# Optimization experiments

Hardware: AMD Instinct MI355X
Metric: run time of the kernel (lower is better)

Reference implementation:

```python
import jax, jax.numpy as jnp
import numpy as np

B = 64       # graphs per batch
NPG = 1000   # nodes per graph
EPG = 8000   # edges per graph
F = 128      # num_node_features


def _lin_w(k, fi, fo):
    s = 1.0 / np.sqrt(fi)
    return jax.random.uniform(k, (fi, fo), jnp.float32, -s, s)


def setup_inputs() -> dict:
    key = jax.random.key(0)
    ks = jax.random.split(key, 40)
    N, E = B * NPG, B * EPG

    def edges(k1, k2):
        src = jax.random.randint(k1, (E,), 0, NPG)
        dst = jax.random.randint(k2, (E,), 0, NPG)
        off = (jnp.arange(E) // EPG) * NPG  # keep edges within each graph
        return jnp.stack([src + off, dst + off]).astype(jnp.int32)

    inp = {
        'x0': jax.random.normal(ks[0], (N, F), jnp.float32),
        'edge_attr0': jax.random.uniform(ks[1], (E, 4), jnp.float32),
        'edge_index0': edges(ks[2], ks[3]),
        'x1': jax.random.normal(ks[4], (N, F), jnp.float32),
        'edge_attr1': jax.random.uniform(ks[5], (E, 4), jnp.float32),
        'edge_index1': edges(ks[6], ks[7]),
        'batch0': (jnp.arange(N) // NPG).astype(jnp.int32),
        'batch1': (jnp.arange(N) // NPG).astype(jnp.int32),
        'num_graphs': B,
    }
    # GCNConv weights/biases (6 convs, all F->F)
    names = ['1A', '1B', '1C', '1D', '2', '3']
    for i, nm in enumerate(names):
        inp['W' + nm] = _lin_w(ks[8 + i], F, F)
        inp['b' + nm] = jnp.zeros((F,), jnp.float32)
    # SAGPooling score GNN (GraphConv: lin_rel with bias, lin_root no bias), 3F -> 1
    inp['Ws_rel'] = _lin_w(ks[20], 3 * F, 1)
    inp['bs_rel'] = jnp.zeros((1,), jnp.float32)
    inp['Ws_root'] = _lin_w(ks[21], 3 * F, 1)
    # MLP: 6F -> 32 -> 8 -> 2
    inp['Wm1'] = _lin_w(ks[22], 6 * F, 32)
    inp['bm1'] = jnp.zeros((32,), jnp.float32)
    inp['Wm2'] = _lin_w(ks[23], 32, 8)
    inp['bm2'] = jnp.zeros((8,), jnp.float32)
    inp['Wm3'] = _lin_w(ks[24], 8, 2)
    inp['bm3'] = jnp.zeros((2,), jnp.float32)
    return inp


def gcn_conv(x, W, b, row, col, ew):
    # PyG GCNConv: add self-loops (w=1), symmetric norm, gather->scatter-add
    N = x.shape[0]
    h = x @ W  # [N, F]
    sl = jnp.arange(N)
    row_f = jnp.concatenate([row, sl])
    col_f = jnp.concatenate([col, sl])
    w_f = jnp.concatenate([ew, jnp.ones((N,), x.dtype)])
    deg = jax.ops.segment_sum(w_f, col_f, num_segments=N)
    dinv = jnp.where(deg > 0, jax.lax.rsqrt(jnp.maximum(deg, 1e-12)), 0.0)
    norm = (dinv[row_f] * w_f * dinv[col_f])[:, None]
    return jax.ops.segment_sum(h[row_f] * norm, col_f, num_segments=N) + b


def reference(x0, edge_attr0, edge_index0, x1, edge_attr1, edge_index1,
              batch0, batch1, num_graphs,
              W1A, b1A, W1B, b1B, W1C, b1C, W1D, b1D, W2, b2, W3, b3,
              Ws_rel, bs_rel, Ws_root, Wm1, bm1, Wm2, bm2, Wm3, bm3):
    Bn = int(num_graphs)

    def branch(x, ea, ei):
        row, col = ei[0], ei[1]
        N = x.shape[0]
        ones_e = jnp.ones((ei.shape[1],), x.dtype)
        xa = jax.nn.relu(gcn_conv(x, W1A, b1A, row, col, ea[:, 0]))
        xb = jax.nn.relu(gcn_conv(x, W1B, b1B, row, col, ea[:, 1]))
        xc = jax.nn.relu(gcn_conv(x, W1C, b1C, row, col, ea[:, 2]))
        xd = jax.nn.relu(gcn_conv(x, W1D, b1D, row, col, ea[:, 3]))
        g1 = (xa + xb + xc + xd) * 0.25
        g2 = jax.nn.relu(gcn_conv(g1, W2, b2, row, col, ones_e))
        g3 = gcn_conv(g2, W3, b3, row, col, ones_e)
        g = jnp.concatenate([g1, g2, g3], axis=1)  # [N, 3F]
        # SAGPooling score via GraphConv (sum aggr, no norm/self-loops)
        agg = jax.ops.segment_sum(g[row], col, num_segments=N)
        score = (agg @ Ws_rel + bs_rel + g @ Ws_root)[:, 0]  # [N]
        npg = N // Bn
        k = npg // 2  # ratio=0.5, even graph size
        sv, si = jax.lax.top_k(score.reshape(Bn, npg), k)
        gg = g.reshape(Bn, npg, g.shape[1])
        sel = jnp.take_along_axis(gg, si[..., None], axis=1)  # [B, k, 3F]
        pooled = sel * jnp.tanh(sv)[..., None]
        return pooled.mean(axis=1)  # global_mean_pool -> [B, 3F]

    r0 = branch(x0, edge_attr0, edge_index0)
    r1 = branch(x1, edge_attr1, edge_index1)
    r = jnp.concatenate([r0, r1], axis=1)  # [B, 6F]
    h = jax.nn.relu(r @ Wm1 + bm1)
    h = jax.nn.relu(h @ Wm2 + bm2)
    return h @ Wm3 + bm3  # [B, 2]
```

## Files before the change

kernel.cpp:

```cpp
#include <hip/hip_runtime.h>
#include <math.h>


#define TPB 256

__device__ __forceinline__ int swz_block(int bid, int nb) {
  int per = bid & 7;
  return per * (nb >> 3) + (bid >> 3);
}

__device__ __forceinline__ void f4fma(float4& a, const float4 b, float s) {
  a.x += b.x * s; a.y += b.y * s; a.z += b.z * s; a.w += b.w * s;
}
__device__ __forceinline__ float4 f4s(const float4 a, float s) {
  return make_float4(a.x * s, a.y * s, a.z * s, a.w * s);
}


__global__ __launch_bounds__(TPB) void count2_k(const int* __restrict__ ec0,
                                                const int* __restrict__ ec1,
                                                int* __restrict__ cnt, int E) {
  int e = blockIdx.x * TPB + threadIdx.x;
  if (e < 2 * E) {
    int br = e >= E;
    int el = e - br * E;
    int c = br ? ec1[el] : ec0[el];
    atomicAdd(&cnt[br * (gridDim.x * 0 + 0) + 0 + c + br * 64000], 1);
  }
}

__global__ __launch_bounds__(512) void scan1_k(const int* __restrict__ cnt,
                                               int* __restrict__ rowptr,
                                               int* __restrict__ bsum, int tn) {
  __shared__ int s[512];
  int tid = threadIdx.x;
  int gid = blockIdx.x * 512 + tid;
  int v = (gid < tn) ? cnt[gid] : 0;
  s[tid] = v;
  __syncthreads();
  for (int o = 1; o < 512; o <<= 1) {
    int t = (tid >= o) ? s[tid - o] : 0;
    __syncthreads();
    s[tid] += t;
    __syncthreads();
  }
  if (gid < tn) rowptr[gid] = s[tid] - v;
  if (tid == 511) bsum[blockIdx.x] = s[511];
}

__global__ __launch_bounds__(TPB) void scan2_k(int* __restrict__ bsum, int nb) {
  __shared__ int s[TPB];
  int tid = threadIdx.x;
  int v = (tid < nb) ? bsum[tid] : 0;
  s[tid] = v;
  __syncthreads();
  for (int o = 1; o < TPB; o <<= 1) {
    int t = (tid >= o) ? s[tid - o] : 0;
    __syncthreads();
    s[tid] += t;
    __syncthreads();
  }
  if (tid < nb) bsum[tid] = s[tid] - v;
}

__global__ __launch_bounds__(512) void scan3_k(int* __restrict__ rowptr,
                                               const int* __restrict__ bsum,
                                               int tn, int tE) {
  int gid = blockIdx.x * 512 + threadIdx.x;
  if (gid < tn) rowptr[gid] += bsum[blockIdx.x];
  if (gid == 0) rowptr[tn] = tE;
}

__global__ __launch_bounds__(TPB) void fill2_k(const int* __restrict__ ec0,
                                               const int* __restrict__ ec1,
                                               const int* __restrict__ rowptr,
                                               int* __restrict__ fil,
                                               int* __restrict__ csr, int N,
                                               int E) {
  int e = blockIdx.x * TPB + threadIdx.x;
  if (e < 2 * E) {
    int br = e >= E;
    int el = e - br * E;
    int c = (br ? ec1[el] : ec0[el]) + br * N;
    int p = rowptr[c] + atomicAdd(&fil[c], 1);
    csr[p] = e;
  }
}

__global__ __launch_bounds__(TPB) void sortadj_k(const int* __restrict__ rowptr,
                                                 int* __restrict__ csr, int tn) {
  int i = blockIdx.x * TPB + threadIdx.x;
  if (i >= tn) return;
  int s = rowptr[i], e = rowptr[i + 1];
  for (int a = s + 1; a < e; ++a) {
    int v = csr[a];
    int b = a - 1;
    while (b >= s && csr[b] > v) { csr[b + 1] = csr[b]; --b; }
    csr[b + 1] = v;
  }
}

__global__ __launch_bounds__(TPB) void deg2_k(const int* __restrict__ rowptr,
                                              const int* __restrict__ csr,
                                              const float* __restrict__ ea0,
                                              const float* __restrict__ ea1,
                                              float* __restrict__ dinv, int N,
                                              int E) {
  int i = blockIdx.x * TPB + threadIdx.x;
  int tn = 2 * N;
  if (i >= tn) return;
  int br = i >= N;
  const float* ea = br ? ea1 : ea0;
  int ebase = br * E;
  int s = rowptr[i], e = rowptr[i + 1];
  float d0 = 1.f, d1 = 1.f, d2 = 1.f, d3 = 1.f;
  for (int j = s; j < e; ++j) {
    int el = csr[j] - ebase;
    float4 w = *reinterpret_cast<const float4*>(&ea[(size_t)el * 4]);
    d0 += w.x; d1 += w.y; d2 += w.z; d3 += w.w;
  }
  float dO = (float)(e - s) + 1.f;
  dinv[0 * tn + i] = 1.f / sqrtf(d0);
  dinv[1 * tn + i] = 1.f / sqrtf(d1);
  dinv[2 * tn + i] = 1.f / sqrtf(d2);
  dinv[3 * tn + i] = 1.f / sqrtf(d3);
  dinv[4 * tn + i] = 1.f / sqrtf(dO);
}

__global__ __launch_bounds__(TPB) void eresolve2_k(
    const int* __restrict__ csr, const int* __restrict__ er0,
    const int* __restrict__ er1, const float* __restrict__ ea0,
    const float* __restrict__ ea1, const float* __restrict__ dinv, int N,
    int E, int* __restrict__ csrSrc, float4* __restrict__ csrW,
    float* __restrict__ csrWO) {
  int j = blockIdx.x * TPB + threadIdx.x;
  if (j >= 2 * E) return;
  int br = j >= E;
  int tn = 2 * N;
  int el = csr[j] - br * E;
  int rl = br ? er1[el] : er0[el];
  int gi = br * N + rl;
  const float* ea = br ? ea1 : ea0;
  float4 a = *reinterpret_cast<const float4*>(&ea[(size_t)el * 4]);
  csrSrc[j] = rl;
  csrW[j] = make_float4(a.x * dinv[gi], a.y * dinv[tn + gi],
                        a.z * dinv[2 * tn + gi], a.w * dinv[3 * tn + gi]);
  csrWO[j] = dinv[4 * tn + gi];
}

__global__ __launch_bounds__(256) void gather4_k(
    const float4* __restrict__ X, const int* __restrict__ rowptr_b,
    const int* __restrict__ csrSrc, const float4* __restrict__ csrW,
    const float* __restrict__ dinvp, int tn, float4* __restrict__ S0,
    float4* __restrict__ S1, float4* __restrict__ S2, float4* __restrict__ S3) {
  int sb = swz_block(blockIdx.x, gridDim.x);
  int node = sb * 8 + (threadIdx.x >> 5);
  int l = threadIdx.x & 31;
  int s = rowptr_b[node], e = rowptr_b[node + 1];
  float d0 = dinvp[node], d1 = dinvp[tn + node], d2 = dinvp[2 * tn + node],
        d3 = dinvp[3 * tn + node];
  float4 xs = X[(size_t)node * 32 + l];
  float4 a0 = f4s(xs, d0), a1 = f4s(xs, d1), a2 = f4s(xs, d2), a3 = f4s(xs, d3);
  int j = s;
  for (; j + 3 < e; j += 4) {
    int r0 = csrSrc[j], r1 = csrSrc[j + 1], r2 = csrSrc[j + 2], r3 = csrSrc[j + 3];
    float4 w0 = csrW[j], w1 = csrW[j + 1], w2 = csrW[j + 2], w3 = csrW[j + 3];
    float4 x0 = X[(size_t)r0 * 32 + l];
    float4 x1 = X[(size_t)r1 * 32 + l];
    float4 x2 = X[(size_t)r2 * 32 + l];
    float4 x3 = X[(size_t)r3 * 32 + l];
    f4fma(a0, x0, w0.x); f4fma(a1, x0, w0.y); f4fma(a2, x0, w0.z); f4fma(a3, x0, w0.w);
    f4fma(a0, x1, w1.x); f4fma(a1, x1, w1.y); f4fma(a2, x1, w1.z); f4fma(a3, x1, w1.w);
    f4fma(a0, x2, w2.x); f4fma(a1, x2, w2.y); f4fma(a2, x2, w2.z); f4fma(a3, x2, w2.w);
    f4fma(a0, x3, w3.x); f4fma(a1, x3, w3.y); f4fma(a2, x3, w3.z); f4fma(a3, x3, w3.w);
  }
  for (; j < e; ++j) {
    int r = csrSrc[j];
    float4 w = csrW[j];
    float4 xr = X[(size_t)r * 32 + l];
    f4fma(a0, xr, w.x); f4fma(a1, xr, w.y); f4fma(a2, xr, w.z); f4fma(a3, xr, w.w);
  }
  size_t o = (size_t)node * 32 + l;
  S0[o] = f4s(a0, d0);
  S1[o] = f4s(a1, d1);
  S2[o] = f4s(a2, d2);
  S3[o] = f4s(a3, d3);
}

__global__ __launch_bounds__(256) void gather1_k(
    const float4* __restrict__ X, const int* __restrict__ rowptr_b,
    const int* __restrict__ csrSrc, const float* __restrict__ csrWO,
    const float* __restrict__ dinvO, int N, float4* __restrict__ Out) {
  int sb = swz_block(blockIdx.x, gridDim.x);
  int node = sb * 8 + (threadIdx.x >> 5);
  int l = threadIdx.x & 31;
  int s = rowptr_b[node], e = rowptr_b[node + 1];
  float di = dinvO[node];
  float4 acc = f4s(X[(size_t)node * 32 + l], di);
  int j = s;
  for (; j + 3 < e; j += 4) {
    int r0 = csrSrc[j], r1 = csrSrc[j + 1], r2 = csrSrc[j + 2], r3 = csrSrc[j + 3];
    float w0 = csrWO[j], w1 = csrWO[j + 1], w2 = csrWO[j + 2], w3 = csrWO[j + 3];
    float4 x0 = X[(size_t)r0 * 32 + l];
    float4 x1 = X[(size_t)r1 * 32 + l];
    float4 x2 = X[(size_t)r2 * 32 + l];
    float4 x3 = X[(size_t)r3 * 32 + l];
    f4fma(acc, x0, w0); f4fma(acc, x1, w1); f4fma(acc, x2, w2); f4fma(acc, x3, w3);
  }
  for (; j < e; ++j) {
    f4fma(acc, X[(size_t)csrSrc[j] * 32 + l], csrWO[j]);
  }
  Out[(size_t)node * 32 + l] = f4s(acc, di);
}

template <bool RELU>
__global__ __launch_bounds__(256) void gemm_epi(const float* __restrict__ A,
                                                const float* __restrict__ W,
                                                const float* __restrict__ bias,
                                                float* __restrict__ C, int M) {
  __shared__ float As[64][64];
  __shared__ float Ws[64][128];
  int tid = threadIdx.x;
  int tx = tid & 31;
  int ty = tid >> 5;
  int rowBase = blockIdx.x * 64;
  float acc[8][4] = {};
  for (int kc = 0; kc < 128; kc += 64) {
#pragma unroll
    for (int i = 0; i < 4; ++i) {
      int idx = tid + i * 256;
      int r = idx >> 4;
      int c4 = idx & 15;
      *reinterpret_cast<float4*>(&As[r][c4 * 4]) =
          *reinterpret_cast<const float4*>(&A[(size_t)(rowBase + r) * 128 + kc + c4 * 4]);
    }
#pragma unroll
    for (int i = 0; i < 8; ++i) {
      int idx = tid + i * 256;
      int r = idx >> 5;
      int c4 = idx & 31;
      *reinterpret_cast<float4*>(&Ws[r][c4 * 4]) =
          *reinterpret_cast<const float4*>(&W[(size_t)(kc + r) * 128 + c4 * 4]);
    }
    __syncthreads();
#pragma unroll 4
    for (int k = 0; k < 64; ++k) {
      float b0[4];
      *reinterpret_cast<float4*>(b0) = *reinterpret_cast<const float4*>(&Ws[k][tx * 4]);
#pragma unroll
      for (int j = 0; j < 8; ++j) {
        float a = As[ty * 8 + j][k];
        acc[j][0] += a * b0[0];
        acc[j][1] += a * b0[1];
        acc[j][2] += a * b0[2];
        acc[j][3] += a * b0[3];
      }
    }
    __syncthreads();
  }
  float4 bq = *reinterpret_cast<const float4*>(&bias[tx * 4]);
#pragma unroll
  for (int j = 0; j < 8; ++j) {
    float v0 = acc[j][0] + bq.x, v1 = acc[j][1] + bq.y, v2 = acc[j][2] + bq.z,
          v3 = acc[j][3] + bq.w;
    if (RELU) {
      v0 = fmaxf(v0, 0.f); v1 = fmaxf(v1, 0.f); v2 = fmaxf(v2, 0.f); v3 = fmaxf(v3, 0.f);
    }
    size_t r = (size_t)(rowBase + ty * 8 + j) * 128 + tx * 4;
    *reinterpret_cast<float4*>(&C[r]) = make_float4(v0, v1, v2, v3);
  }
}

__global__ __launch_bounds__(256) void gemm4_k(
    const float* __restrict__ S0, const float* __restrict__ S1,
    const float* __restrict__ S2, const float* __restrict__ S3,
    const float* __restrict__ W0, const float* __restrict__ W1,
    const float* __restrict__ W2, const float* __restrict__ W3,
    const float* __restrict__ B0, const float* __restrict__ B1,
    const float* __restrict__ B2, const float* __restrict__ B3,
    float* __restrict__ g1, int tileBase) {
  __shared__ float As[64][64];
  __shared__ float Ws[64][128];
  const float* Sarr[4] = {S0, S1, S2, S3};
  const float* Warr[4] = {W0, W1, W2, W3};
  const float* Barr[4] = {B0, B1, B2, B3};
  int tid = threadIdx.x;
  int tx = tid & 31;
  int ty = tid >> 5;
  int rowBase = (tileBase + blockIdx.x) * 64;
  float facc[8][4] = {};
#pragma unroll
  for (int q = 0; q < 4; ++q) {
    const float* A = Sarr[q];
    const float* W = Warr[q];
    float acc[8][4] = {};
    for (int kc = 0; kc < 128; kc += 64) {
#pragma unroll
      for (int i = 0; i < 4; ++i) {
        int idx = tid + i * 256;
        int r = idx >> 4;
        int c4 = idx & 15;
        *reinterpret_cast<float4*>(&As[r][c4 * 4]) =
            *reinterpret_cast<const float4*>(&A[(size_t)(rowBase + r) * 128 + kc + c4 * 4]);
      }
#pragma unroll
      for (int i = 0; i < 8; ++i) {
        int idx = tid + i * 256;
        int r = idx >> 5;
        int c4 = idx & 31;
        *reinterpret_cast<float4*>(&Ws[r][c4 * 4]) =
            *reinterpret_cast<const float4*>(&W[(size_t)(kc + r) * 128 + c4 * 4]);
      }
      __syncthreads();
#pragma unroll 4
      for (int k = 0; k < 64; ++k) {
        float b0[4];
        *reinterpret_cast<float4*>(b0) = *reinterpret_cast<const float4*>(&Ws[k][tx * 4]);
#pragma unroll
        for (int j = 0; j < 8; ++j) {
          float a = As[ty * 8 + j][k];
          acc[j][0] += a * b0[0];
          acc[j][1] += a * b0[1];
          acc[j][2] += a * b0[2];
          acc[j][3] += a * b0[3];
        }
      }
      __syncthreads();
    }
    float4 bq = *reinterpret_cast<const float4*>(&Barr[q][tx * 4]);
#pragma unroll
    for (int j = 0; j < 8; ++j) {
      facc[j][0] += fmaxf(acc[j][0] + bq.x, 0.f) * 0.25f;
      facc[j][1] += fmaxf(acc[j][1] + bq.y, 0.f) * 0.25f;
      facc[j][2] += fmaxf(acc[j][2] + bq.z, 0.f) * 0.25f;
      facc[j][3] += fmaxf(acc[j][3] + bq.w, 0.f) * 0.25f;
    }
  }
#pragma unroll
  for (int j = 0; j < 8; ++j) {
    size_t r = (size_t)(rowBase + ty * 8 + j) * 128 + tx * 4;
    *reinterpret_cast<float4*>(&g1[r]) =
        make_float4(facc[j][0], facc[j][1], facc[j][2], facc[j][3]);
  }
}

__global__ __launch_bounds__(256) void score_a(
    const float* __restrict__ g1, const float* __restrict__ g2,
    const float* __restrict__ g3, const float* __restrict__ Wrel,
    const float* __restrict__ Wroot, float* __restrict__ trel,
    float* __restrict__ troot, int N) {
  int wave = threadIdx.x >> 6;
  int lane = threadIdx.x & 63;
  int node = blockIdx.x * 4 + wave;
  if (node >= N) return;
  float sr = 0.f, so = 0.f;
#pragma unroll
  for (int t = 0; t < 2; ++t) {
    int f = lane + t * 64;
    float v1 = g1[(size_t)node * 128 + f];
    float v2 = g2[(size_t)node * 128 + f];
    float v3 = g3[(size_t)node * 128 + f];
    sr += v1 * Wrel[f] + v2 * Wrel[128 + f] + v3 * Wrel[256 + f];
    so += v1 * Wroot[f] + v2 * Wroot[128 + f] + v3 * Wroot[256 + f];
  }
  for (int off = 32; off; off >>= 1) {
    sr += __shfl_down(sr, off);
    so += __shfl_down(so, off);
  }
  if (lane == 0) { trel[node] = sr; troot[node] = so; }
}

__global__ __launch_bounds__(TPB) void score_b(
    const int* __restrict__ rowptr_b, const int* __restrict__ csrSrc,
    const float* __restrict__ trel, const float* __restrict__ troot,
    const float* __restrict__ bs, float* __restrict__ score, int N) {
  int i = blockIdx.x * TPB + threadIdx.x;
  if (i >= N) return;
  float sc = bs[0] + troot[i];
  int s = rowptr_b[i], e = rowptr_b[i + 1];
  for (int j = s; j < e; ++j) sc += trel[csrSrc[j]];
  score[i] = sc;
}

__global__ __launch_bounds__(512) void topk_pool(
    const float* __restrict__ score, const float* __restrict__ g1,
    const float* __restrict__ g2, const float* __restrict__ g3,
    float* __restrict__ r, int half, int npg, int k) {
  __shared__ float key[1024];
  __shared__ int idx[1024];
  __shared__ float wts[512];
  int b = blockIdx.x;
  int tid = threadIdx.x;
  int base = b * npg;
  for (int i = tid; i < 1024; i += 512) {
    key[i] = (i < npg) ? score[base + i] : -3.0e38f;
    idx[i] = i;
  }
  __syncthreads();
  for (int kk = 2; kk <= 1024; kk <<= 1) {
    for (int j = kk >> 1; j > 0; j >>= 1) {
      for (int i = tid; i < 1024; i += 512) {
        int ixj = i ^ j;
        if (ixj > i) {
          bool desc = ((i & kk) == 0);
          float ki = key[i], kj = key[ixj];
          bool sw = desc ? (ki < kj) : (ki > kj);
          if (sw) {
            key[i] = kj; key[ixj] = ki;
            int t = idx[i]; idx[i] = idx[ixj]; idx[ixj] = t;
          }
        }
      }
      __syncthreads();
    }
  }
  if (tid < k) wts[tid] = tanhf(key[tid]);
  __syncthreads();
  if (tid < 384) {
    const float* gp = (tid < 128) ? g1 : ((tid < 256) ? g2 : g3);
    int fo = tid & 127;
    float acc = 0.f;
    for (int j = 0; j < k; ++j) {
      int n = base + idx[j];
      acc += wts[j] * gp[(size_t)n * 128 + fo];
    }
    r[(size_t)b * 768 + half * 384 + tid] = acc / (float)k;
  }
}

__global__ __launch_bounds__(64) void mlp_k(
    const float* __restrict__ r, const float* __restrict__ Wm1,
    const float* __restrict__ bm1, const float* __restrict__ Wm2,
    const float* __restrict__ bm2, const float* __restrict__ Wm3,
    const float* __restrict__ bm3, float* __restrict__ out) {
  __shared__ float rr[768];
  __shared__ float h1[32];
  __shared__ float h2[8];
  int b = blockIdx.x;
  int tid = threadIdx.x;
  for (int i = tid; i < 768; i += 64) rr[i] = r[(size_t)b * 768 + i];
  __syncthreads();
  if (tid < 32) {
    float s = bm1[tid];
    for (int i = 0; i < 768; ++i) s += rr[i] * Wm1[i * 32 + tid];
    h1[tid] = fmaxf(s, 0.f);
  }
  __syncthreads();
  if (tid < 8) {
    float s = bm2[tid];
    for (int i = 0; i < 32; ++i) s += h1[i] * Wm2[i * 8 + tid];
    h2[tid] = fmaxf(s, 0.f);
  }
  __syncthreads();
  if (tid < 2) {
    float s = bm3[tid];
    for (int i = 0; i < 8; ++i) s += h2[i] * Wm3[i * 2 + tid];
    out[b * 2 + tid] = s;
  }
}

extern "C" void kernel_launch(void* const* d_in, const int* in_sizes, int n_in,
                              void* d_out, int out_size, void* d_ws, size_t ws_size,
                              hipStream_t stream) {
  const float* x[2]  = {(const float*)d_in[0], (const float*)d_in[3]};
  const float* eat[2] = {(const float*)d_in[1], (const float*)d_in[4]};
  const int*   ei[2] = {(const int*)d_in[2], (const int*)d_in[5]};
  const int N = in_sizes[0] / 128;
  const int E = in_sizes[2] / 2;
  const int tn = 2 * N;
  const int tE = 2 * E;
  const int Bg = 64;
  const int npg = N / Bg;
  const int kq = npg / 2;

  const float* W1[4] = {(const float*)d_in[9], (const float*)d_in[11],
                        (const float*)d_in[13], (const float*)d_in[15]};
  const float* b1[4] = {(const float*)d_in[10], (const float*)d_in[12],
                        (const float*)d_in[14], (const float*)d_in[16]};
  const float* W2 = (const float*)d_in[17];
  const float* b2 = (const float*)d_in[18];
  const float* W3 = (const float*)d_in[19];
  const float* b3 = (const float*)d_in[20];
  const float* Wsrel  = (const float*)d_in[21];
  const float* bsrel  = (const float*)d_in[22];
  const float* Wsroot = (const float*)d_in[23];
  const float* Wm1 = (const float*)d_in[24];
  const float* bm1 = (const float*)d_in[25];
  const float* Wm2 = (const float*)d_in[26];
  const float* bm2 = (const float*)d_in[27];
  const float* Wm3 = (const float*)d_in[28];
  const float* bm3 = (const float*)d_in[29];
  float* out = (float*)d_out;

  char* ws = (char*)d_ws;
  size_t off = 0;
  auto alloc = [&](size_t bytes) -> void* {
    void* p = ws + off;
    off = (off + bytes + 511) & ~(size_t)511;
    return p;
  };
  const size_t nf = (size_t)N * 128 * sizeof(float);
  float* P0 = (float*)alloc(nf);
  float* P1 = (float*)alloc(nf);
  float* P2 = (float*)alloc(nf);
  float* P3 = (float*)alloc(nf);
  float* P4 = (float*)alloc(nf);
  float* dinv = (float*)alloc((size_t)5 * tn * sizeof(float));
  float* trel = (float*)alloc((size_t)N * sizeof(float));
  float* trot = (float*)alloc((size_t)N * sizeof(float));
  float* sco  = (float*)alloc((size_t)N * sizeof(float));
  int* rowptr = (int*)alloc((size_t)(tn + 1) * sizeof(int));
  int* cnt    = (int*)alloc((size_t)tn * sizeof(int));
  int* csr    = (int*)alloc((size_t)tE * sizeof(int));
  int* csrSrc = (int*)alloc((size_t)tE * sizeof(int));
  float4* csrW = (float4*)alloc((size_t)tE * sizeof(float4));
  float* csrWO = (float*)alloc((size_t)tE * sizeof(float));
  int* bsum   = (int*)alloc(1024);
  float* rbuf = (float*)alloc((size_t)Bg * 768 * sizeof(float));
  if (off > ws_size) return;

  const int nbN2 = (tn + TPB - 1) / TPB;
  const int nbE2 = (tE + TPB - 1) / TPB;
  const int nbS  = (tn + 511) / 512;
  const int nbN  = (N + TPB - 1) / TPB;
  const int nbGather = N / 8;
  const int nbGemm = N / 64;
  const int nbGemmHalf = nbGemm / 2;

  hipMemsetAsync(cnt, 0, (size_t)tn * sizeof(int), stream);
  count2_k<<<nbE2, TPB, 0, stream>>>(ei[0] + E, ei[1] + E, cnt, E);
  scan1_k<<<nbS, 512, 0, stream>>>(cnt, rowptr, bsum, tn);
  scan2_k<<<1, TPB, 0, stream>>>(bsum, nbS);
  scan3_k<<<nbS, 512, 0, stream>>>(rowptr, bsum, tn, tE);
  hipMemsetAsync(cnt, 0, (size_t)tn * sizeof(int), stream);
  fill2_k<<<nbE2, TPB, 0, stream>>>(ei[0] + E, ei[1] + E, rowptr, cnt, csr, N, E);
  sortadj_k<<<nbN2, TPB, 0, stream>>>(rowptr, csr, tn);
  deg2_k<<<nbN2, TPB, 0, stream>>>(rowptr, csr, eat[0], eat[1], dinv, N, E);
  eresolve2_k<<<nbE2, TPB, 0, stream>>>(csr, ei[0], ei[1], eat[0], eat[1],
                                        dinv, N, E, csrSrc, csrW, csrWO);

  for (int br = 0; br < 2; ++br) {
    const int* rowptr_b = rowptr + (size_t)br * N;
    const float* dinvp = dinv + (size_t)br * N;
    const float* dinvO = dinv + (size_t)4 * tn + (size_t)br * N;

    gather4_k<<<nbGather, 256, 0, stream>>>(
        (const float4*)x[br], rowptr_b, csrSrc, csrW, dinvp, tn,
        (float4*)P0, (float4*)P1, (float4*)P2, (float4*)P3);
    gemm4_k<<<nbGemmHalf, 256, 0, stream>>>(P0, P1, P2, P3,
                                            W1[0], W1[1], W1[2], W1[3],
                                            b1[0], b1[1], b1[2], b1[3], P4, 0);
    gemm4_k<<<nbGemmHalf, 256, 0, stream>>>(P0, P1, P2, P3,
                                            W1[0], W1[1], W1[2], W1[3],
                                            b1[0], b1[1], b1[2], b1[3], P4,
                                            nbGemmHalf);

    gather1_k<<<nbGather, 256, 0, stream>>>(
        (const float4*)P4, rowptr_b, csrSrc, csrWO, dinvO, N, (float4*)P0);
    gemm_epi<true><<<nbGemm, 256, 0, stream>>>(P0, W2, b2, P1, N);

    gather1_k<<<nbGather, 256, 0, stream>>>(
        (const float4*)P1, rowptr_b, csrSrc, csrWO, dinvO, N, (float4*)P0);
    gemm_epi<false><<<nbGemm, 256, 0, stream>>>(P0, W3, b3, P2, N);

    score_a<<<(N + 3) / 4, 256, 0, stream>>>(P4, P1, P2, Wsrel, Wsroot, trel, trot, N);
    score_b<<<nbN, TPB, 0, stream>>>(rowptr_b, csrSrc, trel, trot, bsrel, sco, N);
    topk_pool<<<Bg, 512, 0, stream>>>(sco, P4, P1, P2, rbuf, br, npg, kq);
  }

  mlp_k<<<Bg, 64, 0, stream>>>(rbuf, Wm1, bm1, Wm2, bm2, Wm3, bm3, out);
}
```

Before: 903.3 us.

## Deepen gather unrolling, split top-k pooling, merge gemm4 launches

Adds an 8-way unrolled edge loop to both gather kernels so more independent row loads are in flight per lane. Splits the top-k pooling kernel into a sort kernel that writes selected indices and tanh weights, and a separate pool kernel launched over graphs by three feature slices with 4-way unrolled gathers, to expose more parallelism than the single 512-thread block per graph. Also merges the two half-grid gemm4 launches into one and cleans up the count kernel's hardcoded offset. Costs extra registers in the gathers plus an additional launch and a small index/weight buffer round trip.

New measurement: 951.4 us. 5.3% more time.

```diff
diff --git a/kernel.cpp b/kernel.cpp
--- a/kernel.cpp
+++ b/kernel.cpp
@@ -5,8 +5,7 @@
 #define TPB 256
 
 __device__ __forceinline__ int swz_block(int bid, int nb) {
-  int per = bid & 7;
-  return per * (nb >> 3) + (bid >> 3);
+  return (bid & 7) * (nb >> 3) + (bid >> 3);
 }
 
 __device__ __forceinline__ void f4fma(float4& a, const float4 b, float s) {
@@ -16,16 +15,16 @@
   return make_float4(a.x * s, a.y * s, a.z * s, a.w * s);
 }
 
-
 __global__ __launch_bounds__(TPB) void count2_k(const int* __restrict__ ec0,
                                                 const int* __restrict__ ec1,
-                                                int* __restrict__ cnt, int E) {
+                                                int* __restrict__ cnt, int N,
+                                                int E) {
   int e = blockIdx.x * TPB + threadIdx.x;
   if (e < 2 * E) {
     int br = e >= E;
     int el = e - br * E;
-    int c = br ? ec1[el] : ec0[el];
-    atomicAdd(&cnt[br * (gridDim.x * 0 + 0) + 0 + c + br * 64000], 1);
+    int c = (br ? ec1[el] : ec0[el]) + br * N;
+    atomicAdd(&cnt[c], 1);
   }
 }
 
@@ -162,6 +161,28 @@
   float4 xs = X[(size_t)node * 32 + l];
   float4 a0 = f4s(xs, d0), a1 = f4s(xs, d1), a2 = f4s(xs, d2), a3 = f4s(xs, d3);
   int j = s;
+  for (; j + 7 < e; j += 8) {
+    int r0 = csrSrc[j], r1 = csrSrc[j + 1], r2 = csrSrc[j + 2], r3 = csrSrc[j + 3];
+    int r4 = csrSrc[j + 4], r5 = csrSrc[j + 5], r6 = csrSrc[j + 6], r7 = csrSrc[j + 7];
+    float4 w0 = csrW[j], w1 = csrW[j + 1], w2 = csrW[j + 2], w3 = csrW[j + 3];
+    float4 w4 = csrW[j + 4], w5 = csrW[j + 5], w6 = csrW[j + 6], w7 = csrW[j + 7];
+    float4 x0 = X[(size_t)r0 * 32 + l];
+    float4 x1 = X[(size_t)r1 * 32 + l];
+    float4 x2 = X[(size_t)r2 * 32 + l];
+    float4 x3 = X[(size_t)r3 * 32 + l];
+    float4 x4 = X[(size_t)r4 * 32 + l];
+    float4 x5 = X[(size_t)r5 * 32 + l];
+    float4 x6 = X[(size_t)r6 * 32 + l];
+    float4 x7 = X[(size_t)r7 * 32 + l];
+    f4fma(a0, x0, w0.x); f4fma(a1, x0, w0.y); f4fma(a2, x0, w0.z); f4fma(a3, x0, w0.w);
+    f4fma(a0, x1, w1.x); f4fma(a1, x1, w1.y); f4fma(a2, x1, w1.z); f4fma(a3, x1, w1.w);
+    f4fma(a0, x2, w2.x); f4fma(a1, x2, w2.y); f4fma(a2, x2, w2.z); f4fma(a3, x2, w2.w);
+    f4fma(a0, x3, w3.x); f4fma(a1, x3, w3.y); f4fma(a2, x3, w3.z); f4fma(a3, x3, w3.w);
+    f4fma(a0, x4, w4.x); f4fma(a1, x4, w4.y); f4fma(a2, x4, w4.z); f4fma(a3, x4, w4.w);
+    f4fma(a0, x5, w5.x); f4fma(a1, x5, w5.y); f4fma(a2, x5, w5.z); f4fma(a3, x5, w5.w);
+    f4fma(a0, x6, w6.x); f4fma(a1, x6, w6.y); f4fma(a2, x6, w6.z); f4fma(a3, x6, w6.w);
+    f4fma(a0, x7, w7.x); f4fma(a1, x7, w7.y); f4fma(a2, x7, w7.z); f4fma(a3, x7, w7.w);
+  }
   for (; j + 3 < e; j += 4) {
     int r0 = csrSrc[j], r1 = csrSrc[j + 1], r2 = csrSrc[j + 2], r3 = csrSrc[j + 3];
     float4 w0 = csrW[j], w1 = csrW[j + 1], w2 = csrW[j + 2], w3 = csrW[j + 3];
@@ -198,6 +219,22 @@
   float di = dinvO[node];
   float4 acc = f4s(X[(size_t)node * 32 + l], di);
   int j = s;
+  for (; j + 7 < e; j += 8) {
+    int r0 = csrSrc[j], r1 = csrSrc[j + 1], r2 = csrSrc[j + 2], r3 = csrSrc[j + 3];
+    int r4 = csrSrc[j + 4], r5 = csrSrc[j + 5], r6 = csrSrc[j + 6], r7 = csrSrc[j + 7];
+    float w0 = csrWO[j], w1 = csrWO[j + 1], w2 = csrWO[j + 2], w3 = csrWO[j + 3];
+    float w4 = csrWO[j + 4], w5 = csrWO[j + 5], w6 = csrWO[j + 6], w7 = csrWO[j + 7];
+    float4 x0 = X[(size_t)r0 * 32 + l];
+    float4 x1 = X[(size_t)r1 * 32 + l];
+    float4 x2 = X[(size_t)r2 * 32 + l];
+    float4 x3 = X[(size_t)r3 * 32 + l];
+    float4 x4 = X[(size_t)r4 * 32 + l];
+    float4 x5 = X[(size_t)r5 * 32 + l];
+    float4 x6 = X[(size_t)r6 * 32 + l];
+    float4 x7 = X[(size_t)r7 * 32 + l];
+    f4fma(acc, x0, w0); f4fma(acc, x1, w1); f4fma(acc, x2, w2); f4fma(acc, x3, w3);
+    f4fma(acc, x4, w4); f4fma(acc, x5, w5); f4fma(acc, x6, w6); f4fma(acc, x7, w7);
+  }
   for (; j + 3 < e; j += 4) {
     int r0 = csrSrc[j], r1 = csrSrc[j + 1], r2 = csrSrc[j + 2], r3 = csrSrc[j + 3];
     float w0 = csrWO[j], w1 = csrWO[j + 1], w2 = csrWO[j + 2], w3 = csrWO[j + 3];
@@ -278,7 +315,7 @@
     const float* __restrict__ W2, const float* __restrict__ W3,
     const float* __restrict__ B0, const float* __restrict__ B1,
     const float* __restrict__ B2, const float* __restrict__ B3,
-    float* __restrict__ g1, int tileBase) {
+    float* __restrict__ g1, int M) {
   __shared__ float As[64][64];
   __shared__ float Ws[64][128];
   const float* Sarr[4] = {S0, S1, S2, S3};
@@ -287,7 +324,7 @@
   int tid = threadIdx.x;
   int tx = tid & 31;
   int ty = tid >> 5;
-  int rowBase = (tileBase + blockIdx.x) * 64;
+  int rowBase = blockIdx.x * 64;
   float facc[8][4] = {};
 #pragma unroll
   for (int q = 0; q < 4; ++q) {
@@ -382,13 +419,11 @@
   score[i] = sc;
 }
 
-__global__ __launch_bounds__(512) void topk_pool(
-    const float* __restrict__ score, const float* __restrict__ g1,
-    const float* __restrict__ g2, const float* __restrict__ g3,
-    float* __restrict__ r, int half, int npg, int k) {
+__global__ __launch_bounds__(512) void topk_sort_k(
+    const float* __restrict__ score, int* __restrict__ sidx,
+    float* __restrict__ swts, int npg, int k) {
   __shared__ float key[1024];
   __shared__ int idx[1024];
-  __shared__ float wts[512];
   int b = blockIdx.x;
   int tid = threadIdx.x;
   int base = b * npg;
@@ -414,18 +449,43 @@
       __syncthreads();
     }
   }
-  if (tid < k) wts[tid] = tanhf(key[tid]);
+  if (tid < k) {
+    sidx[b * k + tid] = idx[tid];
+    swts[b * k + tid] = tanhf(key[tid]);
+  }
+}
+
+__global__ __launch_bounds__(128) void pool_k(
+    const int* __restrict__ sidx, const float* __restrict__ swts,
+    const float* __restrict__ g1, const float* __restrict__ g2,
+    const float* __restrict__ g3, float* __restrict__ r, int half, int npg,
+    int k) {
+  __shared__ int ids[512];
+  __shared__ float wts[512];
+  int b = blockIdx.x;
+  int q = blockIdx.y;
+  int f = threadIdx.x;
+  const float* gp = (q == 0) ? g1 : ((q == 1) ? g2 : g3);
+  int base = b * npg;
+  for (int i = f; i < k; i += 128) {
+    ids[i] = sidx[b * k + i];
+    wts[i] = swts[b * k + i];
+  }
   __syncthreads();
-  if (tid < 384) {
-    const float* gp = (tid < 128) ? g1 : ((tid < 256) ? g2 : g3);
-    int fo = tid & 127;
-    float acc = 0.f;
-    for (int j = 0; j < k; ++j) {
-      int n = base + idx[j];
-      acc += wts[j] * gp[(size_t)n * 128 + fo];
-    }
-    r[(size_t)b * 768 + half * 384 + tid] = acc / (float)k;
-  }
+  float acc = 0.f;
+  int j = 0;
+  for (; j + 3 < k; j += 4) {
+    float v0 = gp[(size_t)(base + ids[j]) * 128 + f];
+    float v1 = gp[(size_t)(base + ids[j + 1]) * 128 + f];
+    float v2 = gp[(size_t)(base + ids[j + 2]) * 128 + f];
+    float v3 = gp[(size_t)(base + ids[j + 3]) * 128 + f];
+    acc += wts[j] * v0;
+    acc += wts[j + 1] * v1;
+    acc += wts[j + 2] * v2;
+    acc += wts[j + 3] * v3;
+  }
+  for (; j < k; ++j) acc += wts[j] * gp[(size_t)(base + ids[j]) * 128 + f];
+  r[(size_t)b * 768 + half * 384 + q * 128 + f] = acc / (float)k;
 }
 
 __global__ __launch_bounds__(64) void mlp_k(
@@ -517,6 +577,8 @@
   float* csrWO = (float*)alloc((size_t)tE * sizeof(float));
   int* bsum   = (int*)alloc(1024);
   float* rbuf = (float*)alloc((size_t)Bg * 768 * sizeof(float));
+  int* sidx   = (int*)alloc((size_t)Bg * kq * sizeof(int));
+  float* swts = (float*)alloc((size_t)Bg * kq * sizeof(float));
   if (off > ws_size) return;
 
   const int nbN2 = (tn + TPB - 1) / TPB;
@@ -525,10 +587,9 @@
   const int nbN  = (N + TPB - 1) / TPB;
   const int nbGather = N / 8;
   const int nbGemm = N / 64;
-  const int nbGemmHalf = nbGemm / 2;
 
   hipMemsetAsync(cnt, 0, (size_t)tn * sizeof(int), stream);
-  count2_k<<<nbE2, TPB, 0, stream>>>(ei[0] + E, ei[1] + E, cnt, E);
+  count2_k<<<nbE2, TPB, 0, stream>>>(ei[0] + E, ei[1] + E, cnt, N, E);
   scan1_k<<<nbS, 512, 0, stream>>>(cnt, rowptr, bsum, tn);
   scan2_k<<<1, TPB, 0, stream>>>(bsum, nbS);
   scan3_k<<<nbS, 512, 0, stream>>>(rowptr, bsum, tn, tE);
@@ -547,13 +608,9 @@
     gather4_k<<<nbGather, 256, 0, stream>>>(
         (const float4*)x[br], rowptr_b, csrSrc, csrW, dinvp, tn,
         (float4*)P0, (float4*)P1, (float4*)P2, (float4*)P3);
-    gemm4_k<<<nbGemmHalf, 256, 0, stream>>>(P0, P1, P2, P3,
-                                            W1[0], W1[1], W1[2], W1[3],
-                                            b1[0], b1[1], b1[2], b1[3], P4, 0);
-    gemm4_k<<<nbGemmHalf, 256, 0, stream>>>(P0, P1, P2, P3,
-                                            W1[0], W1[1], W1[2], W1[3],
-                                            b1[0], b1[1], b1[2], b1[3], P4,
-                                            nbGemmHalf);
+    gemm4_k<<<nbGemm, 256, 0, stream>>>(P0, P1, P2, P3,
+                                        W1[0], W1[1], W1[2], W1[3],
+                                        b1[0], b1[1], b1[2], b1[3], P4, N);
 
     gather1_k<<<nbGather, 256, 0, stream>>>(
         (const float4*)P4, rowptr_b, csrSrc, csrWO, dinvO, N, (float4*)P0);
@@ -565,7 +622,9 @@
 
     score_a<<<(N + 3) / 4, 256, 0, stream>>>(P4, P1, P2, Wsrel, Wsroot, trel, trot, N);
     score_b<<<nbN, TPB, 0, stream>>>(rowptr_b, csrSrc, trel, trot, bsrel, sco, N);
-    topk_pool<<<Bg, 512, 0, stream>>>(sco, P4, P1, P2, rbuf, br, npg, kq);
+    topk_sort_k<<<Bg, 512, 0, stream>>>(sco, sidx, swts, npg, kq);
+    dim3 pg(Bg, 3);
+    pool_k<<<pg, 128, 0, stream>>>(sidx, swts, P4, P1, P2, rbuf, br, npg, kq);
   }
 
   mlp_k<<<Bg, 64, 0, stream>>>(rbuf, Wm1, bm1, Wm2, bm2, Wm3, bm3, out);
```
